# Optimization experiments

Hardware: AMD Instinct MI355X
Metric: run time of the kernel (lower is better)

## Reference

```python
import jax, jax.numpy as jnp
import numpy as np

B, C, N = 8, 512, 8192
H = 8
D = C // H
HID = int(C * 2.0)
EPS_ATTN = 1e-6
EPS_BN = 1e-5


def setup_inputs() -> dict:
    key = jax.random.key(0)
    ks = jax.random.split(key, 8)
    sc = lambda fan_in: 1.0 / np.sqrt(fan_in)
    return {
        "x": jax.random.normal(ks[0], (B, C, N), dtype=jnp.float32),
        # qkv Linear: stored [in, out] for x @ W
        "qkv_w": jax.random.normal(ks[1], (C, 3 * C), dtype=jnp.float32) * sc(C),
        "qkv_b": jnp.zeros((3 * C,), dtype=jnp.float32),
        "proj_w": jax.random.normal(ks[2], (C, C), dtype=jnp.float32) * sc(C),
        "proj_b": jnp.zeros((C,), dtype=jnp.float32),
        # FFN conv1x1 (no bias, BN follows)
        "w1": jax.random.normal(ks[3], (HID, C), dtype=jnp.float32) * sc(C),
        "g1": jnp.ones((HID,), dtype=jnp.float32),
        "b1": jnp.zeros((HID,), dtype=jnp.float32),
        "w2": jax.random.normal(ks[4], (C, HID), dtype=jnp.float32) * sc(HID),
        "g2": jnp.ones((C,), dtype=jnp.float32),
        "b2": jnp.zeros((C,), dtype=jnp.float32),
    }


def _phi(x):
    # elu(x) + 1  (strictly positive kernel feature map)
    return jax.nn.elu(x) + 1.0


def _bn(x, gamma, beta):
    # training-mode BatchNorm1d over [B, C, N]: stats over (batch, spatial)
    mean = jnp.mean(x, axis=(0, 2), keepdims=True)
    var = jnp.var(x, axis=(0, 2), keepdims=True)
    xh = (x - mean) * jax.lax.rsqrt(var + EPS_BN)
    return xh * gamma[None, :, None] + beta[None, :, None]


def reference(x, qkv_w, qkv_b, proj_w, proj_b, w1, g1, b1, w2, g2, b2):
    # ---- linear attention ----
    xt = jnp.swapaxes(x, 1, 2)                       # [B, N, C]
    qkv = xt @ qkv_w + qkv_b                         # [B, N, 3C]
    q, k, v = jnp.split(qkv, 3, axis=-1)
    reshape_h = lambda t: jnp.swapaxes(t.reshape(B, N, H, D), 1, 2)  # [B, H, N, D]
    q, k, v = reshape_h(q), reshape_h(k), reshape_h(v)
    q_phi = _phi(q)
    k_phi = _phi(k)
    S = jnp.einsum("bhnd,bhne->bhde", k_phi, v)      # K^T V, [B,H,D,D]
    k_sum = k_phi.sum(axis=-2)                       # [B,H,D]
    numer = jnp.einsum("bhnd,bhde->bhne", q_phi, S)  # [B,H,N,D]
    denom = jnp.einsum("bhnd,bhd->bhn", q_phi, k_sum)[..., None] + EPS_ATTN
    out = numer / denom                              # [B,H,N,D]
    out = jnp.swapaxes(out, 1, 2).reshape(B, N, C)
    out = out @ proj_w + proj_b                      # [B, N, C]
    y = jnp.swapaxes(out, 1, 2)                      # [B, C, N]
    # ---- attention residual ----
    x = x + y
    # ---- FFN: conv1x1 -> BN -> ReLU, twice ----
    h = jnp.einsum("oc,bcn->bon", w1, x)             # [B, HID, N]
    h = jax.nn.relu(_bn(h, g1, b1))
    h = jnp.einsum("oc,bcn->bon", w2, h)             # [B, C, N]
    h = jax.nn.relu(_bn(h, g2, b2))
    return x + h
```

## Files before the change

kernel.cpp:

```cpp
#include <hip/hip_runtime.h>
#include <hip/hip_bf16.h>

#define B_    8
#define C_    512
#define N_    8192
#define H_    8
#define D_    64
#define HID_  1024

constexpr float EPS_ATTN = 1e-6f;
constexpr float EPS_BN   = 1e-5f;

typedef _Float16 half8 __attribute__((ext_vector_type(8)));
typedef _Float16 half4 __attribute__((ext_vector_type(4)));
typedef float    floatx4 __attribute__((ext_vector_type(4)));

#define GLOAD_LDS(gp, lp) \
  __builtin_amdgcn_global_load_lds((const __attribute__((address_space(1))) void*)(gp), \
                                   (__attribute__((address_space(3))) void*)(lp), 16, 0, 0)

template<int EPI>
__global__ __launch_bounds__(256)
void gemm_mfma(const _Float16* __restrict__ Abase, size_t a_bstride,
               const _Float16* __restrict__ Wt, int K,
               float* __restrict__ OUTf, size_t outf_bs,
               _Float16* __restrict__ OUTh, size_t outh_bs,
               const float* __restrict__ bias,
               const float* __restrict__ resid, size_t res_bs,
               int phi_limit)
{
    __shared__ _Float16 Al0[4096], Al1[4096];
    __shared__ _Float16 Bl0[4096], Bl1[4096];

    const int tid = threadIdx.x;
    const int b = blockIdx.z;
    const int n_base = blockIdx.x * 128;
    const int o_base = blockIdx.y * 128;
    const int w = tid >> 6, l = tid & 63;
    const int wm = w >> 1, wn = w & 1;

    const _Float16* A  = Abase + (size_t)b * a_bstride + (size_t)n_base * K;
    const _Float16* Bw = Wt + (size_t)o_base * K;

    const int r0 = tid & 127;
    const int s0 = tid >> 7;
    const _Float16* ga0 = A  + (size_t)r0 * K + s0 * 8;
    const _Float16* ga1 = A  + (size_t)r0 * K + (2 + s0) * 8;
    const _Float16* gb0 = Bw + (size_t)r0 * K + s0 * 8;
    const _Float16* gb1 = Bw + (size_t)r0 * K + (2 + s0) * 8;
    const int loff = (tid & 192) * 8;

    floatx4 acc[4][4];
    #pragma unroll
    for (int mi = 0; mi < 4; ++mi)
        #pragma unroll
        for (int ni = 0; ni < 4; ++ni)
            acc[mi][ni] = (floatx4){0.f, 0.f, 0.f, 0.f};

    const int s = l >> 4;
    const int r = l & 15;

    auto stage = [&](_Float16* AlB, _Float16* BlB, int c0) {
        GLOAD_LDS(ga0 + c0, AlB + loff);
        GLOAD_LDS(ga1 + c0, AlB + 2048 + loff);
        GLOAD_LDS(gb0 + c0, BlB + loff);
        GLOAD_LDS(gb1 + c0, BlB + 2048 + loff);
    };
    auto compute = [&](const _Float16* AlB, const _Float16* BlB) {
        half8 af[4], bf[4];
        #pragma unroll
        for (int f = 0; f < 4; ++f) {
            af[f] = *(const half8*)&AlB[(size_t)(s * 128 + wm * 64 + f * 16 + r) * 8];
            bf[f] = *(const half8*)&BlB[(size_t)(s * 128 + wn * 64 + f * 16 + r) * 8];
        }
        #pragma unroll
        for (int mi = 0; mi < 4; ++mi)
            #pragma unroll
            for (int ni = 0; ni < 4; ++ni)
                acc[mi][ni] = __builtin_amdgcn_mfma_f32_16x16x32_f16(af[mi], bf[ni], acc[mi][ni], 0, 0, 0);
    };

    const int NT = K >> 5;
    stage(Al0, Bl0, 0);
    __syncthreads();
    for (int t = 0; t < NT; t += 2) {
        stage(Al1, Bl1, (t + 1) << 5);
        compute(Al0, Bl0);
        __syncthreads();
        if (t + 2 < NT) stage(Al0, Bl0, (t + 2) << 5);
        compute(Al1, Bl1);
        __syncthreads();
    }

    #pragma unroll
    for (int mi = 0; mi < 4; ++mi) {
        const int n_g = n_base + wm * 64 + mi * 16 + ((l >> 4) << 2);
        #pragma unroll
        for (int ni = 0; ni < 4; ++ni) {
            const int o_g = o_base + wn * 64 + ni * 16 + (l & 15);
            floatx4 v = acc[mi][ni];
            if (EPI == 1 || EPI == 2) {
                const float bi = bias[o_g];
                v[0] += bi; v[1] += bi; v[2] += bi; v[3] += bi;
            }
            if (EPI == 1) {
                if (o_g < phi_limit) {
                    #pragma unroll
                    for (int j = 0; j < 4; ++j)
                        v[j] = v[j] > 0.f ? v[j] + 1.f : __expf(v[j]);
                }
            }
            if (EPI == 2) {
                const float4 rv = *(const float4*)(resid + (size_t)b * res_bs + (size_t)o_g * N_ + n_g);
                v[0] += rv.x; v[1] += rv.y; v[2] += rv.z; v[3] += rv.w;
                *(floatx4*)(OUTf + (size_t)b * outf_bs + (size_t)o_g * N_ + n_g) = v;
            } else {
                half4 hv;
                #pragma unroll
                for (int j = 0; j < 4; ++j) hv[j] = (_Float16)v[j];
                *(half4*)(OUTh + (size_t)b * outh_bs + (size_t)o_g * N_ + n_g) = hv;
            }
        }
    }
}

template<bool INF16, bool AFFINE>
__global__ __launch_bounds__(256)
void cvtT(const void* __restrict__ src, _Float16* __restrict__ dst,
          int R, int Cc, size_t sbs, size_t dbs,
          const float* __restrict__ scale, const float* __restrict__ shift)
{
    __shared__ _Float16 t[64][76];
    const int tid = threadIdx.x;
    const int b = blockIdx.z;
    const int c0 = blockIdx.x * 64;
    const int r0 = blockIdx.y * 64;
    const int rl = tid >> 3;
    const int cg = (tid & 7) * 8;
    #pragma unroll
    for (int hh = 0; hh < 2; ++hh) {
        const int rr = rl + hh * 32;
        float vals[8];
        if (INF16) {
            const _Float16* sp = (const _Float16*)src + (size_t)b * sbs + (size_t)(r0 + rr) * Cc + c0 + cg;
            const half8 hv = *(const half8*)sp;
            #pragma unroll
            for (int j = 0; j < 8; ++j) vals[j] = (float)hv[j];
        } else {
            const float* sp = (const float*)src + (size_t)b * sbs + (size_t)(r0 + rr) * Cc + c0 + cg;
            const float4 v0 = *(const float4*)sp;
            const float4 v1 = *(const float4*)(sp + 4);
            vals[0] = v0.x; vals[1] = v0.y; vals[2] = v0.z; vals[3] = v0.w;
            vals[4] = v1.x; vals[5] = v1.y; vals[6] = v1.z; vals[7] = v1.w;
        }
        if (AFFINE) {
            const float sc = scale[r0 + rr], sf = shift[r0 + rr];
            #pragma unroll
            for (int j = 0; j < 8; ++j) vals[j] = fmaxf(fmaf(vals[j], sc, sf), 0.f);
        }
        #pragma unroll
        for (int j = 0; j < 8; ++j) t[rr][cg + j] = (_Float16)vals[j];
    }
    __syncthreads();
    const int cl = tid >> 3;
    const int rg = (tid & 7) * 8;
    #pragma unroll
    for (int hh = 0; hh < 2; ++hh) {
        const int cc = cl + hh * 32;
        half8 o;
        #pragma unroll
        for (int j = 0; j < 8; ++j) o[j] = t[rg + j][cc];
        *(half8*)(dst + (size_t)b * dbs + (size_t)(c0 + cc) * R + r0 + rg) = o;
    }
}

__global__ __launch_bounds__(256)
void cast_f16(const float* __restrict__ in, _Float16* __restrict__ out, int n4)
{
    const int i = blockIdx.x * 256 + threadIdx.x;
    if (i < n4) {
        const float4 v = *(const float4*)(in + (size_t)i * 4);
        half4 h; h[0] = (_Float16)v.x; h[1] = (_Float16)v.y; h[2] = (_Float16)v.z; h[3] = (_Float16)v.w;
        *(half4*)(out + (size_t)i * 4) = h;
    }
}

__global__ __launch_bounds__(256)
void attn_kv_mfma(const _Float16* __restrict__ qkvh,
                  float* __restrict__ S_part, float* __restrict__ ks_part)
{
    __shared__ _Float16 kt0[2048], kt1[2048], vt0[2048], vt1[2048];
    const int tid = threadIdx.x;
    const int bh = blockIdx.y;
    const int b = bh >> 3, h = bh & 7;
    const size_t kbase = ((size_t)b * 1536 + 512  + h * 64) * N_;
    const size_t vbase = ((size_t)b * 1536 + 1024 + h * 64) * N_;
    const int n0 = blockIdx.x * 1024;
    const int w = tid >> 6, l = tid & 63;

    const int rr = tid & 63, ss = tid >> 6;
    const _Float16* gk = qkvh + kbase + (size_t)rr * N_ + n0 + ss * 8;
    const _Float16* gv = qkvh + vbase + (size_t)rr * N_ + n0 + ss * 8;
    const int loff = (tid & 192) * 8;

    floatx4 acc[4], accks;
    #pragma unroll
    for (int ni = 0; ni < 4; ++ni) acc[ni] = (floatx4){0.f, 0.f, 0.f, 0.f};
    accks = (floatx4){0.f, 0.f, 0.f, 0.f};

    const int s = l >> 4, r = l & 15;
    const int drow = w * 16 + r;
    half8 onesv;
    #pragma unroll
    for (int j = 0; j < 8; ++j) onesv[j] = (_Float16)1.0f;

    auto stage = [&](_Float16* kB, _Float16* vB, int nt) {
        GLOAD_LDS(gk + nt, kB + loff);
        GLOAD_LDS(gv + nt, vB + loff);
    };
    auto compute = [&](const _Float16* kB, const _Float16* vB) {
        const half8 af = *(const half8*)&kB[(size_t)(s * 64 + drow) * 8];
        half8 bf[4];
        #pragma unroll
        for (int ni = 0; ni < 4; ++ni)
            bf[ni] = *(const half8*)&vB[(size_t)(s * 64 + ni * 16 + r) * 8];
        #pragma unroll
        for (int ni = 0; ni < 4; ++ni)
            acc[ni] = __builtin_amdgcn_mfma_f32_16x16x32_f16(af, bf[ni], acc[ni], 0, 0, 0);
        accks = __builtin_amdgcn_mfma_f32_16x16x32_f16(af, onesv, accks, 0, 0, 0);
    };

    stage(kt0, vt0, 0);
    __syncthreads();
    for (int t = 0; t < 32; t += 2) {
        stage(kt1, vt1, (t + 1) * 32);
        compute(kt0, vt0);
        __syncthreads();
        if (t + 2 < 32) stage(kt0, vt0, (t + 2) * 32);
        compute(kt1, vt1);
        __syncthreads();
    }

    float* Sp = S_part + ((size_t)blockIdx.x * 64 + bh) * 4096;
    #pragma unroll
    for (int ni = 0; ni < 4; ++ni)
        #pragma unroll
        for (int j = 0; j < 4; ++j)
            Sp[(w * 16 + s * 4 + j) * 64 + ni * 16 + r] = acc[ni][j];
    if (r == 0) {
        float* kp = ks_part + ((size_t)blockIdx.x * 64 + bh) * 64;
        #pragma unroll
        for (int j = 0; j < 4; ++j) kp[w * 16 + s * 4 + j] = accks[j];
    }
}

__global__ __launch_bounds__(256)
void attn_reduce(const float* __restrict__ S_part, const float* __restrict__ ks_part,
                 float* __restrict__ S, float* __restrict__ ksum)
{
    const int bh = blockIdx.x;
    const int tid = threadIdx.x;
    for (int i = tid; i < 4096; i += 256) {
        float s = 0.f;
        #pragma unroll
        for (int c = 0; c < 8; ++c) s += S_part[((size_t)c * 64 + bh) * 4096 + i];
        S[(size_t)bh * 4096 + i] = s;
    }
    if (tid < 64) {
        float s = 0.f;
        #pragma unroll
        for (int c = 0; c < 8; ++c) s += ks_part[((size_t)c * 64 + bh) * 64 + tid];
        ksum[bh * 64 + tid] = s;
    }
}

__global__ __launch_bounds__(256)
void attn_apply_f16(const _Float16* __restrict__ qkvh, const float* __restrict__ S,
                    const float* __restrict__ ksum, _Float16* __restrict__ attnb)
{
    const int tid = threadIdx.x;
    const int bh = blockIdx.y;
    const int b = bh >> 3, h = bh & 7;
    const int n = blockIdx.x * 256 + tid;
    const _Float16* __restrict__ qb = qkvh + ((size_t)b * 1536 + h * 64) * N_ + n;
    const float* __restrict__ Sb = S + (size_t)bh * 4096;
    const float* __restrict__ ks = ksum + bh * 64;
    float acc[64];
    #pragma unroll
    for (int e = 0; e < 64; ++e) acc[e] = 0.f;
    float den = EPS_ATTN;
    for (int d = 0; d < 64; ++d) {
        const float qd = (float)qb[(size_t)d * N_];
        den = fmaf(qd, ks[d], den);
        #pragma unroll
        for (int e = 0; e < 64; ++e)
            acc[e] = fmaf(qd, Sb[d * 64 + e], acc[e]);
    }
    const float inv = 1.0f / den;
    _Float16* __restrict__ ob = attnb + ((size_t)b * N_ + n) * C_ + h * 64;
    #pragma unroll
    for (int g = 0; g < 8; ++g) {
        half8 hv;
        #pragma unroll
        for (int j = 0; j < 8; ++j) hv[j] = (_Float16)(acc[g * 8 + j] * inv);
        *(half8*)(ob + g * 8) = hv;
    }
}

__global__ __launch_bounds__(256)
void bn_stats_h(const _Float16* __restrict__ X, size_t bstride,
                const float* __restrict__ gamma, const float* __restrict__ beta,
                float* __restrict__ scale, float* __restrict__ shift)
{
    const int ch = blockIdx.x;
    const int tid = threadIdx.x;
    double s = 0.0, s2 = 0.0;
    for (int b = 0; b < B_; ++b) {
        const _Float16* base = X + (size_t)b * bstride + (size_t)ch * N_;
        for (int i = tid; i < N_ / 8; i += 256) {
            const half8 v = *(const half8*)(base + (size_t)i * 8);
            #pragma unroll
            for (int j = 0; j < 8; ++j) {
                const float f = (float)v[j];
                s += (double)f; s2 += (double)f * (double)f;
            }
        }
    }
    __shared__ double sh[256], sh2[256];
    sh[tid] = s; sh2[tid] = s2;
    __syncthreads();
    for (int off = 128; off > 0; off >>= 1) {
        if (tid < off) { sh[tid] += sh[tid + off]; sh2[tid] += sh2[tid + off]; }
        __syncthreads();
    }
    if (tid == 0) {
        const double n = (double)B_ * (double)N_;
        const double mean = sh[0] / n;
        const double var  = sh2[0] / n - mean * mean;
        const double inv  = 1.0 / sqrt(var + (double)EPS_BN);
        const double g = (double)gamma[ch];
        scale[ch] = (float)(g * inv);
        shift[ch] = (float)((double)beta[ch] - mean * g * inv);
    }
}

__global__ __launch_bounds__(256)
void final_add_h(float* __restrict__ out, const _Float16* __restrict__ h2,
                 const float* __restrict__ scale, const float* __restrict__ shift)
{
    const size_t i = (size_t)blockIdx.x * 256 + threadIdx.x;
    const int c = (int)((i >> 10) & (C_ - 1));
    const float sc = scale[c], sf = shift[c];
    const half8 hv = *(const half8*)(h2 + i * 8);
    float4 x0 = ((float4*)out)[i * 2];
    float4 x1 = ((float4*)out)[i * 2 + 1];
    x0.x += fmaxf(fmaf((float)hv[0], sc, sf), 0.f);
    x0.y += fmaxf(fmaf((float)hv[1], sc, sf), 0.f);
    x0.z += fmaxf(fmaf((float)hv[2], sc, sf), 0.f);
    x0.w += fmaxf(fmaf((float)hv[3], sc, sf), 0.f);
    x1.x += fmaxf(fmaf((float)hv[4], sc, sf), 0.f);
    x1.y += fmaxf(fmaf((float)hv[5], sc, sf), 0.f);
    x1.z += fmaxf(fmaf((float)hv[6], sc, sf), 0.f);
    x1.w += fmaxf(fmaf((float)hv[7], sc, sf), 0.f);
    ((float4*)out)[i * 2] = x0;
    ((float4*)out)[i * 2 + 1] = x1;
}

extern "C" void kernel_launch(void* const* d_in, const int* in_sizes, int n_in,
                              void* d_out, int out_size, void* d_ws, size_t ws_size,
                              hipStream_t stream)
{
    const float* x      = (const float*)d_in[0];
    const float* qkv_w  = (const float*)d_in[1];
    const float* qkv_b  = (const float*)d_in[2];
    const float* proj_w = (const float*)d_in[3];
    const float* proj_b = (const float*)d_in[4];
    const float* w1     = (const float*)d_in[5];
    const float* g1     = (const float*)d_in[6];
    const float* b1     = (const float*)d_in[7];
    const float* w2     = (const float*)d_in[8];
    const float* g2     = (const float*)d_in[9];
    const float* b2     = (const float*)d_in[10];
    float* out = (float*)d_out;

    const size_t MB = 1ull << 20;
    char* ws = (char*)d_ws;
    _Float16* qkvh   = (_Float16*)ws;
    _Float16* h16    = (_Float16*)ws;
    _Float16* h2h    = (_Float16*)(ws + 128 * MB);
    float*    S_part = (float*)(ws + 192 * MB);
    float*    ks_part= (float*)(ws + 200 * MB);
    float*    S      = (float*)(ws + 201 * MB);
    float*    ksum   = (float*)(ws + 202 * MB);
    _Float16* ht     = (_Float16*)(ws + 192 * MB);
    _Float16* xb     = (_Float16*)(ws + 320 * MB);
    _Float16* attnb  = xb;
    _Float16* x1b    = xb;
    _Float16* qkvwT  = (_Float16*)(ws + 384 * MB);
    _Float16* projwT = qkvwT + 1536 * 512;
    _Float16* w1h    = projwT + 512 * 512;
    _Float16* w2h    = w1h + 1024 * 512;
    float* scale1 = (float*)(w2h + 512 * 1024);
    float* shift1 = scale1 + 1024;
    float* scale2 = shift1 + 1024;
    float* shift2 = scale2 + 512;

    const size_t xbs = (size_t)C_ * N_;

    cvtT<false, false><<<dim3(24, 8, 1), 256, 0, stream>>>(qkv_w, qkvwT, 512, 1536, 0, 0, nullptr, nullptr);
    cvtT<false, false><<<dim3(8, 8, 1), 256, 0, stream>>>(proj_w, projwT, 512, 512, 0, 0, nullptr, nullptr);
    cast_f16<<<512, 256, 0, stream>>>(w1, w1h, 131072);
    cast_f16<<<512, 256, 0, stream>>>(w2, w2h, 131072);

    cvtT<false, false><<<dim3(128, 8, 8), 256, 0, stream>>>(x, xb, 512, 8192, xbs, (size_t)N_ * C_, nullptr, nullptr);

    gemm_mfma<1><<<dim3(64, 12, 8), 256, 0, stream>>>(
        xb, (size_t)N_ * 512, qkvwT, 512,
        nullptr, 0, qkvh, (size_t)1536 * N_, qkv_b, nullptr, 0, 1024);

    attn_kv_mfma<<<dim3(8, 64), 256, 0, stream>>>(qkvh, S_part, ks_part);
    attn_reduce<<<64, 256, 0, stream>>>(S_part, ks_part, S, ksum);
    attn_apply_f16<<<dim3(32, 64), 256, 0, stream>>>(qkvh, S, ksum, attnb);

    gemm_mfma<2><<<dim3(64, 4, 8), 256, 0, stream>>>(
        attnb, (size_t)N_ * 512, projwT, 512,
        out, xbs, nullptr, 0, proj_b, x, xbs, 0);

    cvtT<false, false><<<dim3(128, 8, 8), 256, 0, stream>>>(out, x1b, 512, 8192, xbs, (size_t)N_ * C_, nullptr, nullptr);

    gemm_mfma<0><<<dim3(64, 8, 8), 256, 0, stream>>>(
        x1b, (size_t)N_ * 512, w1h, 512,
        nullptr, 0, h16, (size_t)HID_ * N_, nullptr, nullptr, 0, 0);

    bn_stats_h<<<1024, 256, 0, stream>>>(h16, (size_t)HID_ * N_, g1, b1, scale1, shift1);

    cvtT<true, true><<<dim3(128, 16, 8), 256, 0, stream>>>(
        h16, ht, 1024, 8192, (size_t)HID_ * N_, (size_t)N_ * HID_, scale1, shift1);

    gemm_mfma<0><<<dim3(64, 4, 8), 256, 0, stream>>>(
        ht, (size_t)N_ * 1024, w2h, 1024,
        nullptr, 0, h2h, xbs, nullptr, nullptr, 0, 0);

    bn_stats_h<<<512, 256, 0, stream>>>(h2h, xbs, g2, b2, scale2, shift2);

    final_add_h<<<16384, 256, 0, stream>>>(out, h2h, scale2, shift2);
}
```

Baseline: 1.173 ms.

## Triple-buffer LDS staging with explicit vmcnt waits in GEMM and KV kernels

Replaces the double-buffered global-to-LDS pipeline in the MFMA GEMM and the attention KV kernel with a three-stage ring buffer. Partial s_waitcnt vmcnt counts let two tiles stay in flight while the current one is computed, instead of a full drain at every __syncthreads. This is meant to hide more global load latency behind the MFMA work. It uses 1.5x the LDS per block, which may lower occupancy, and correctness depends on the hand-counted vmcnt values matching the loads each stage issues.

```diff
diff --git a/kernel.cpp b/kernel.cpp
--- a/kernel.cpp
+++ b/kernel.cpp
@@ -18,6 +18,9 @@
 #define GLOAD_LDS(gp, lp) \
   __builtin_amdgcn_global_load_lds((const __attribute__((address_space(1))) void*)(gp), \
                                    (__attribute__((address_space(3))) void*)(lp), 16, 0, 0)
+
+#define WAITV(N)  asm volatile("s_waitcnt vmcnt(" #N ")" ::: "memory")
+#define MEMFENCE  asm volatile("" ::: "memory")
 
 template<int EPI>
 __global__ __launch_bounds__(256)
@@ -29,8 +32,8 @@
                const float* __restrict__ resid, size_t res_bs,
                int phi_limit)
 {
-    __shared__ _Float16 Al0[4096], Al1[4096];
-    __shared__ _Float16 Bl0[4096], Bl1[4096];
+    __shared__ _Float16 Al[3 * 4096];
+    __shared__ _Float16 Bl[3 * 4096];
 
     const int tid = threadIdx.x;
     const int b = blockIdx.z;
@@ -81,15 +84,22 @@
     };
 
     const int NT = K >> 5;
-    stage(Al0, Bl0, 0);
-    __syncthreads();
-    for (int t = 0; t < NT; t += 2) {
-        stage(Al1, Bl1, (t + 1) << 5);
-        compute(Al0, Bl0);
-        __syncthreads();
-        if (t + 2 < NT) stage(Al0, Bl0, (t + 2) << 5);
-        compute(Al1, Bl1);
-        __syncthreads();
+    _Float16 *pa0 = Al, *pa1 = Al + 4096, *pa2 = Al + 8192;
+    _Float16 *pb0 = Bl, *pb1 = Bl + 4096, *pb2 = Bl + 8192;
+
+    stage(pa0, pb0, 0);
+    stage(pa1, pb1, 32);
+    for (int t = 0; t < NT; ++t) {
+        if (t + 2 < NT) { stage(pa2, pb2, (t + 2) << 5); WAITV(8); }
+        else if (t + 1 < NT) { WAITV(4); }
+        else { WAITV(0); }
+        __builtin_amdgcn_s_barrier();
+        MEMFENCE;
+        compute(pa0, pb0);
+        MEMFENCE;
+        __builtin_amdgcn_s_barrier();
+        _Float16* ta = pa0; pa0 = pa1; pa1 = pa2; pa2 = ta;
+        _Float16* tb = pb0; pb0 = pb1; pb1 = pb2; pb2 = tb;
     }
 
     #pragma unroll
@@ -189,7 +199,7 @@
 void attn_kv_mfma(const _Float16* __restrict__ qkvh,
                   float* __restrict__ S_part, float* __restrict__ ks_part)
 {
-    __shared__ _Float16 kt0[2048], kt1[2048], vt0[2048], vt1[2048];
+    __shared__ _Float16 kt[3 * 2048], vt[3 * 2048];
     const int tid = threadIdx.x;
     const int bh = blockIdx.y;
     const int b = bh >> 3, h = bh & 7;
@@ -230,15 +240,21 @@
         accks = __builtin_amdgcn_mfma_f32_16x16x32_f16(af, onesv, accks, 0, 0, 0);
     };
 
-    stage(kt0, vt0, 0);
-    __syncthreads();
-    for (int t = 0; t < 32; t += 2) {
-        stage(kt1, vt1, (t + 1) * 32);
-        compute(kt0, vt0);
-        __syncthreads();
-        if (t + 2 < 32) stage(kt0, vt0, (t + 2) * 32);
-        compute(kt1, vt1);
-        __syncthreads();
+    _Float16 *pk0 = kt, *pk1 = kt + 2048, *pk2 = kt + 4096;
+    _Float16 *pv0 = vt, *pv1 = vt + 2048, *pv2 = vt + 4096;
+    stage(pk0, pv0, 0);
+    stage(pk1, pv1, 32);
+    for (int t = 0; t < 32; ++t) {
+        if (t + 2 < 32) { stage(pk2, pv2, (t + 2) * 32); WAITV(4); }
+        else if (t + 1 < 32) { WAITV(2); }
+        else { WAITV(0); }
+        __builtin_amdgcn_s_barrier();
+        MEMFENCE;
+        compute(pk0, pv0);
+        MEMFENCE;
+        __builtin_amdgcn_s_barrier();
+        _Float16* tk = pk0; pk0 = pk1; pk1 = pk2; pk2 = tk;
+        _Float16* tv = pv0; pv0 = pv1; pv1 = pv2; pv2 = tv;
     }
 
     float* Sp = S_part + ((size_t)blockIdx.x * 64 + bh) * 4096;
```

After: 1.176 ms. No clear change (+0.3%).
